# Kernel optimization log

Hardware: AMD Instinct MI355X
Metric: run time of the kernel (lower is better)

The kernel has to match this reference:

```python
import jax, jax.numpy as jnp
import numpy as np

H = W = 9
C = 16
D = 34
NHEAD = 2
HDIM = D // NHEAD  # 17
FF = 2048
NLAYERS = 2
EPS = 1e-5


def setup_inputs() -> dict:
    key = jax.random.key(0)
    ks = jax.random.split(key, 16)
    s = 0.05
    return {
        "obs": jax.random.normal(ks[0], (2, H, W), dtype=jnp.float32),
        "conv1_w": jax.random.normal(ks[1], (16, 2, 3, 3), dtype=jnp.float32) * s,
        "conv1_b": jnp.zeros((16,), jnp.float32),
        "conv2_w": jax.random.normal(ks[2], (16, 16, 3, 3), dtype=jnp.float32) * s,
        "conv2_b": jnp.zeros((16,), jnp.float32),
        "in_proj_w": jax.random.normal(ks[3], (NLAYERS, 3 * D, D), dtype=jnp.float32) * s,
        "in_proj_b": jnp.zeros((NLAYERS, 3 * D), jnp.float32),
        "out_proj_w": jax.random.normal(ks[4], (NLAYERS, D, D), dtype=jnp.float32) * s,
        "out_proj_b": jnp.zeros((NLAYERS, D), jnp.float32),
        "lin1_w": jax.random.normal(ks[5], (NLAYERS, FF, D), dtype=jnp.float32) * s,
        "lin1_b": jnp.zeros((NLAYERS, FF), jnp.float32),
        "lin2_w": jax.random.normal(ks[6], (NLAYERS, D, FF), dtype=jnp.float32) * s,
        "lin2_b": jnp.zeros((NLAYERS, D), jnp.float32),
        "ln1_g": jnp.ones((NLAYERS, D), jnp.float32),
        "ln1_b": jnp.zeros((NLAYERS, D), jnp.float32),
        "ln2_g": jnp.ones((NLAYERS, D), jnp.float32),
        "ln2_b": jnp.zeros((NLAYERS, D), jnp.float32),
    }


def _layer_norm(x, g, b):
    m = jnp.mean(x, axis=-1, keepdims=True)
    v = jnp.mean(jnp.square(x - m), axis=-1, keepdims=True)
    return (x - m) * jax.lax.rsqrt(v + EPS) * g + b


def _encoder_layer(x, ipw, ipb, opw, opb, l1w, l1b, l2w, l2b, g1, b1, g2, b2):
    # x: [S, D]. Post-norm TransformerEncoderLayer, eval mode (no dropout).
    S = x.shape[0]
    qkv = x @ ipw.T + ipb  # [S, 3D]
    q, k, v = jnp.split(qkv, 3, axis=-1)
    q = q.reshape(S, NHEAD, HDIM).transpose(1, 0, 2)  # [h, S, d]
    k = k.reshape(S, NHEAD, HDIM).transpose(1, 0, 2)
    v = v.reshape(S, NHEAD, HDIM).transpose(1, 0, 2)
    scores = jnp.einsum("hqd,hkd->hqk", q, k) / jnp.sqrt(jnp.float32(HDIM))
    attn = jax.nn.softmax(scores, axis=-1)
    o = jnp.einsum("hqk,hkd->hqd", attn, v)  # [h, S, d]
    o = o.transpose(1, 0, 2).reshape(S, D)
    o = o @ opw.T + opb
    x = _layer_norm(x + o, g1, b1)
    f = jax.nn.relu(x @ l1w.T + l1b) @ l2w.T + l2b
    return _layer_norm(x + f, g2, b2)


def _conv(x, w, b):
    y = jax.lax.conv_general_dilated(
        x, w, window_strides=(1, 1), padding="SAME",
        dimension_numbers=("NCHW", "OIHW", "NCHW"))
    return jax.nn.relu(y + b[None, :, None, None])


def reference(obs, conv1_w, conv1_b, conv2_w, conv2_b, in_proj_w, in_proj_b,
              out_proj_w, out_proj_b, lin1_w, lin1_b, lin2_w, lin2_b,
              ln1_g, ln1_b, ln2_g, ln2_b):
    x = obs[None]  # [1, 2, H, W]
    x = _conv(x, conv1_w, conv1_b)
    x = _conv(x, conv2_w, conv2_b)
    hw = H * W
    cell_emb = x[0].reshape(C, hw).T  # [hw, C]
    idx = jnp.arange(hw)
    r = (idx // W).astype(jnp.float32)
    c = (idx % W).astype(jnp.float32)
    dx = (r[:, None] - r[None, :]) / ((H - 1) / 2.0)  # [hw, hw]
    dy = (c[:, None] - c[None, :]) / ((W - 1) / 2.0)
    tok_i = jnp.broadcast_to(cell_emb[:, None, :], (hw, hw, C))
    tok_j = jnp.broadcast_to(cell_emb[None, :, :], (hw, hw, C))
    rel = jnp.stack([dx, dy], axis=-1)  # [hw, hw, 2]
    tokens = jnp.concatenate([tok_i, tok_j, rel], axis=-1).reshape(hw * hw, D)
    for l in range(NLAYERS):
        tokens = _encoder_layer(
            tokens, in_proj_w[l], in_proj_b[l], out_proj_w[l], out_proj_b[l],
            lin1_w[l], lin1_b[l], lin2_w[l], lin2_b[l],
            ln1_g[l], ln1_b[l], ln2_g[l], ln2_b[l])
    agent_idx = jnp.argmax(obs[0].reshape(-1))
    start = agent_idx * hw
    agent_tokens = jax.lax.dynamic_slice(tokens, (start, 0), (hw, D))
    return agent_tokens.mean(axis=0)  # [D]
```

## Files before the change

kernel.cpp:

```cpp
#include <hip/hip_runtime.h>
#include <hip/hip_bf16.h>

#define HH 9
#define WW 9
#define HW 81
#define CC 16
#define DD 34
#define SS 6561
#define NHEAD 2
#define HD 17
#define FF 2048
#define EPSF 1e-5f

#define NTILES 52
#define NSPLIT2 26
#define QB 64

#define NIP 7168
#define NOP 3072
#define NW1 131072
#define NW2 98304
#define NLTOT (NIP + NOP + NW1 + NW2)
#define LPREP_BLOCKS 1872
#define NKF 425984
#define NVF 212992
#define NV16 13312
#define ZERO_WORDS 332800
#define ZERO_BLOCKS 1300

#define NEAB 124416
#define NVFL1 12288
#define KSPLIT 8

typedef __attribute__((ext_vector_type(8))) short bf16x8;
typedef __attribute__((ext_vector_type(4))) float f32x4;

__device__ __forceinline__ unsigned short f2b(float f) {
  unsigned int u = __float_as_uint(f);
  u += 0x7fffu + ((u >> 16) & 1u);
  return (unsigned short)(u >> 16);
}

__global__ __launch_bounds__(256) void prep_kernel(
    const float* __restrict__ obs, const float* __restrict__ w1, const float* __restrict__ b1,
    const float* __restrict__ w2, const float* __restrict__ b2,
    float* __restrict__ cell, int* __restrict__ aidx,
    const float* __restrict__ ipw, const float* __restrict__ opw,
    const float* __restrict__ l1w, const float* __restrict__ l2w,
    unsigned short* __restrict__ ipwp, unsigned short* __restrict__ opwp,
    unsigned short* __restrict__ w1p, unsigned short* __restrict__ w2p,
    unsigned short* __restrict__ kfp, unsigned short* __restrict__ vfp,
    float* __restrict__ v16) {
  int bx = blockIdx.x;
  int t = threadIdx.x;
  if (bx == 0) {
    __shared__ float s_obs[2][11][11];
    __shared__ float s_w1[288];
    __shared__ float s_w2[2304];
    __shared__ float s_b1[16], s_b2[16];
    __shared__ float y1[CC][121];
    for (int i = t; i < 2 * 121; i += 256) ((float*)s_obs)[i] = 0.f;
    for (int i = t; i < CC * 121; i += 256) ((float*)y1)[i] = 0.f;
    for (int i = t; i < 288; i += 256) s_w1[i] = w1[i];
    for (int i = t; i < 2304; i += 256) s_w2[i] = w2[i];
    if (t < 16) { s_b1[t] = b1[t]; s_b2[t] = b2[t]; }
    __syncthreads();
    for (int i = t; i < 2 * HW; i += 256) {
      int ic = i / HW, p = i % HW;
      s_obs[ic][1 + p / WW][1 + p % WW] = obs[i];
    }
    __syncthreads();
    if (t == 0) {
      int best = 0; float bv = s_obs[0][1][1];
      for (int p = 1; p < HW; p++) {
        float v = s_obs[0][1 + p / WW][1 + p % WW];
        if (v > bv) { bv = v; best = p; }
      }
      *aidx = best;
    }
    for (int idx = t; idx < CC * HW; idx += 256) {
      int c = idx / HW, p = idx % HW;
      int i = p / WW, j = p % WW;
      float acc = s_b1[c];
#pragma unroll
      for (int ic = 0; ic < 2; ic++)
#pragma unroll
        for (int di = 0; di < 3; di++)
#pragma unroll
          for (int dj = 0; dj < 3; dj++)
            acc += s_obs[ic][i + di][j + dj] * s_w1[((c * 2 + ic) * 3 + di) * 3 + dj];
      y1[c][(i + 1) * 11 + (j + 1)] = fmaxf(acc, 0.f);
    }
    __syncthreads();
    for (int idx = t; idx < CC * HW; idx += 256) {
      int c = idx / HW, p = idx % HW;
      int i = p / WW, j = p % WW;
      float acc = s_b2[c];
#pragma unroll
      for (int ic = 0; ic < CC; ic++)
#pragma unroll
        for (int di = 0; di < 3; di++)
#pragma unroll
          for (int dj = 0; dj < 3; dj++)
            acc += y1[ic][(i + di) * 11 + (j + dj)] * s_w2[((c * CC + ic) * 3 + di) * 3 + dj];
      cell[p * CC + c] = fmaxf(acc, 0.f);
    }
  } else if (bx <= LPREP_BLOCKS) {
    int i = (bx - 1) * 256 + t;
    int layer = i / NLTOT;
    int r = i % NLTOT;
    if (r < NIP) {
      int n = r >> 6, k = r & 63;
      ipwp[layer * NIP + r] =
          (n < 102 && k < DD) ? f2b(ipw[(size_t)layer * 102 * DD + n * DD + k]) : (unsigned short)0;
    } else if (r < NIP + NOP) {
      int rr = r - NIP;
      int n = rr >> 6, k = rr & 63;
      opwp[layer * NOP + rr] =
          (n < DD && k < DD) ? f2b(opw[(size_t)layer * DD * DD + n * DD + k]) : (unsigned short)0;
    } else if (r < NIP + NOP + NW1) {
      int rr = r - NIP - NOP;
      int f = rr >> 6, k = rr & 63;
      w1p[layer * NW1 + rr] =
          (k < DD) ? f2b(l1w[(size_t)layer * FF * DD + f * DD + k]) : (unsigned short)0;
    } else {
      int rr = r - NIP - NOP - NW1;
      int d = rr >> 11, kk = rr & 2047;
      w2p[layer * NW2 + rr] =
          (d < DD) ? f2b(l2w[(size_t)layer * DD * FF + d * FF + kk]) : (unsigned short)0;
    }
  } else {
    int zi = (bx - 1 - LPREP_BLOCKS) * 256 + t;
    if (zi < NKF / 2) ((unsigned int*)kfp)[zi] = 0u;
    else if (zi < NKF / 2 + NVF / 2) ((unsigned int*)vfp)[zi - NKF / 2] = 0u;
    else if (zi < ZERO_WORDS) v16[zi - NKF / 2 - NVF / 2] = 0.f;
  }
}

__global__ __launch_bounds__(256) void ptprep_kernel(
    const float* __restrict__ cell, const float* __restrict__ ipw,
    const float* __restrict__ ipb, float* __restrict__ Pt) {
  int idx = blockIdx.x * 256 + threadIdx.x;
  if (idx >= 2 * HW * 102) return;
  int part = idx / (HW * 102);
  int rem = idx % (HW * 102);
  int a = rem / 102, n = rem % 102;
  float ra = (float)(a / WW) * 0.25f, ca = (float)(a % WW) * 0.25f;
  float acc;
  if (part == 0) {
    acc = ipb[n] + ipw[n * DD + 32] * ra + ipw[n * DD + 33] * ca;
    for (int f = 0; f < CC; f++) acc += ipw[n * DD + f] * cell[a * CC + f];
  } else {
    acc = -(ipw[n * DD + 32] * ra + ipw[n * DD + 33] * ca);
    for (int f = 0; f < CC; f++) acc += ipw[n * DD + CC + f] * cell[a * CC + f];
  }
  Pt[idx] = acc;
}

__global__ __launch_bounds__(256) void expprep_kernel(
    const float* __restrict__ Pt, float* __restrict__ eAB,
    unsigned short* __restrict__ vfragL1) {
  int idx = blockIdx.x * 256 + threadIdx.x;
  const float scale = 0.24253562503633297f;
  if (idx < NEAB) {
    int a = idx % 96; int rest = idx / 96;
    int row = rest % 81; rest /= 81;
    int ab = rest & 1, p = (rest >> 1) & 1, h = rest >> 2;
    float e = 0.f;
    if (a < HW) {
      const float* qrow = Pt + (size_t)ab * (HW * 102) + row * 102 + h * HD;
      const float* krow = Pt + (size_t)p * (HW * 102) + a * 102 + DD + h * HD;
      float dot = 0.f;
#pragma unroll
      for (int d = 0; d < HD; d++) dot += qrow[d] * krow[d];
      e = __expf(fminf(dot * scale, 40.f));
    }
    eAB[idx] = e;
  } else if (idx < NEAB + NVFL1) {
    int j = idx - NEAB;
    int a = j % 96; int rest = j / 96;
    int n = rest % 32; rest /= 32;
    int p = rest & 1, h = rest >> 1;
    float v = 0.f;
    if (a < HW) {
      if (n < HD) v = Pt[(size_t)p * (HW * 102) + a * 102 + 2 * DD + h * HD + n];
      else if (n == HD) v = 1.f;
    }
    vfragL1[((size_t)(h * 2 + p) * 32 + n) * 96 + a] = f2b(v);
  }
}

__global__ __launch_bounds__(256) void fl1_kernel(
    const float* __restrict__ cell, const float* __restrict__ eAB,
    const unsigned short* __restrict__ vfragL1,
    const unsigned short* __restrict__ opwp, const float* __restrict__ opb,
    const float* __restrict__ g1v, const float* __restrict__ b1v,
    const unsigned short* __restrict__ w1p, const unsigned short* __restrict__ w2p,
    const float* __restrict__ fb1, const float* __restrict__ fb2,
    const float* __restrict__ g2v, const float* __restrict__ b2v,
    float* __restrict__ x) {
  __shared__ __align__(16) unsigned short sE[4][16 * 96];
  __shared__ __align__(16) unsigned short soA[16 * 72];
  __shared__ float sxF[16][35];
  __shared__ __align__(16) unsigned short sxA2[16 * 72];
  __shared__ float sxF2[16][35];
  __shared__ __align__(16) unsigned short hw_[4][16 * 40];
  __shared__ float yred[4][16][49];
  int t = threadIdx.x;
  int w = t >> 6, lane = t & 63, quad = lane >> 4, col = lane & 15;
  int r0 = blockIdx.x * 16;
  int nr = min(16, SS - r0);

  for (int i = t; i < 16 * 72; i += 256) { soA[i] = 0; sxA2[i] = 0; }
  for (int i = t; i < 16 * 35; i += 256) { ((float*)sxF)[i] = 0.f; ((float*)sxF2)[i] = 0.f; }
  for (int i = t; i < nr * DD; i += 256) {
    int r = i / DD, d = i - r * DD;
    int row = r0 + r;
    int ii = row / HW, jj = row - ii * HW;
    float v;
    if (d < CC) v = cell[ii * CC + d];
    else if (d < 2 * CC) v = cell[jj * CC + (d - CC)];
    else if (d == 32) v = (float)((ii / WW) - (jj / WW)) * 0.25f;
    else v = (float)((ii % WW) - (jj % WW)) * 0.25f;
    sxF[r][d] = v;
  }

  {
    int h = w >> 1, p = w & 1;
    const float* eA = eAB + ((size_t)((h * 2 + p) * 2 + 0) * 81) * 96;
    const float* eB = eAB + ((size_t)((h * 2 + p) * 2 + 1) * 81) * 96;
    int tl = lane >> 2, asub = lane & 3;
    int row = r0 + tl;
    int tc = row < SS ? row : SS - 1;
    int it = tc / HW, jt = tc - it * HW;
    const float* eAr = eA + it * 96 + asub * 24;
    const float* eBr = eB + jt * 96 + asub * 24;
    unsigned short etmp[24];
#pragma unroll
    for (int k = 0; k < 24; k++) etmp[k] = f2b(eAr[k] * eBr[k]);
    unsigned short* Eb = &sE[w][tl * 96 + asub * 24];
#pragma unroll
    for (int k = 0; k < 3; k++)
      *(bf16x8*)(Eb + k * 8) = *(bf16x8*)(etmp + k * 8);
    const unsigned short* vf = vfragL1 + (size_t)(h * 2 + p) * 32 * 96;
    f32x4 acc0 = {0.f, 0.f, 0.f, 0.f}, acc1 = {0.f, 0.f, 0.f, 0.f};
#pragma unroll
    for (int c = 0; c < 3; c++) {
      bf16x8 ea = *(const bf16x8*)&sE[w][col * 96 + c * 32 + quad * 8];
      bf16x8 vb0 = *(const bf16x8*)&vf[col * 96 + c * 32 + quad * 8];
      bf16x8 vb1 = *(const bf16x8*)&vf[(16 + col) * 96 + c * 32 + quad * 8];
      acc0 = __builtin_amdgcn_mfma_f32_16x16x32_bf16(ea, vb0, acc0, 0, 0, 0);
      acc1 = __builtin_amdgcn_mfma_f32_16x16x32_bf16(ea, vb1, acc1, 0, 0, 0);
    }
    float Sr[4];
#pragma unroll
    for (int r = 0; r < 4; r++) Sr[r] = __shfl(acc1[r], (lane & 48) + 1);
#pragma unroll
    for (int r = 0; r < 4; r++) {
      int rr = quad * 4 + r;
      float inv = 1.f / Sr[r];
      yred[w][rr][col] = acc0[r] * inv;
      if (col == 0) yred[w][rr][16] = acc1[r] * inv;
    }
  }
  __syncthreads();
  for (int i = t; i < 16 * DD; i += 256) {
    int r = i / DD, dd = i - r * DD;
    int h2 = dd / HD, d2 = dd - h2 * HD;
    soA[r * 72 + dd] = f2b(yred[2 * h2][r][d2] + yred[2 * h2 + 1][r][d2]);
  }
  __syncthreads();

  if (w == 0) {
    bf16x8 a0 = *(const bf16x8*)&soA[col * 72 + quad * 8];
    bf16x8 a1 = *(const bf16x8*)&soA[col * 72 + 32 + quad * 8];
    f32x4 y[3];
#pragma unroll
    for (int nt = 0; nt < 3; nt++) {
      int n = nt * 16 + col;
      bf16x8 b0 = *(const bf16x8*)&opwp[n * 64 + quad * 8];
      bf16x8 b1 = *(const bf16x8*)&opwp[n * 64 + 32 + quad * 8];
      f32x4 acc = {0.f, 0.f, 0.f, 0.f};
      acc = __builtin_amdgcn_mfma_f32_16x16x32_bf16(a0, b0, acc, 0, 0, 0);
      y[nt] = __builtin_amdgcn_mfma_f32_16x16x32_bf16(a1, b1, acc, 0, 0, 0);
    }
    float yv[3][4];
    float s1[4] = {0.f, 0.f, 0.f, 0.f}, s2[4] = {0.f, 0.f, 0.f, 0.f};
#pragma unroll
    for (int nt = 0; nt < 3; nt++) {
      int d = nt * 16 + col;
      bool vd = d < DD;
      float ob = vd ? opb[d] : 0.f;
#pragma unroll
      for (int r = 0; r < 4; r++) {
        int row = quad * 4 + r;
        float v = vd ? (y[nt][r] + ob + sxF[row][d]) : 0.f;
        yv[nt][r] = v;
        s1[r] += v;
        s2[r] += v * v;
      }
    }
#pragma unroll
    for (int msk = 1; msk <= 8; msk <<= 1)
#pragma unroll
      for (int r = 0; r < 4; r++) {
        s1[r] += __shfl_xor(s1[r], msk);
        s2[r] += __shfl_xor(s2[r], msk);
      }
#pragma unroll
    for (int r = 0; r < 4; r++) {
      int row = quad * 4 + r;
      float mean = s1[r] * (1.f / DD);
      float var = s2[r] * (1.f / DD) - mean * mean;
      float rs = rsqrtf(var + EPSF);
#pragma unroll
      for (int nt = 0; nt < 3; nt++) {
        int d = nt * 16 + col;
        if (d < DD) {
          float o = (yv[nt][r] - mean) * rs * g1v[d] + b1v[d];
          sxF2[row][d] = o;
          sxA2[row * 72 + d] = f2b(o);
        }
      }
    }
  }
  __syncthreads();

  bf16x8 a0 = *(const bf16x8*)&sxA2[col * 72 + quad * 8];
  bf16x8 a1 = *(const bf16x8*)&sxA2[col * 72 + 32 + quad * 8];
  unsigned short* myh = &hw_[w][0];
  f32x4 acc3[3];
#pragma unroll
  for (int nt = 0; nt < 3; nt++) acc3[nt] = (f32x4){0.f, 0.f, 0.f, 0.f};
  for (int kt = 0; kt < 16; kt++) {
    int fbase = kt * 128 + w * 32;
#pragma unroll
    for (int nt = 0; nt < 2; nt++) {
      int f = fbase + nt * 16 + col;
      bf16x8 b0f = *(const bf16x8*)&w1p[f * 64 + quad * 8];
      bf16x8 b1f = *(const bf16x8*)&w1p[f * 64 + 32 + quad * 8];
      f32x4 hacc = {0.f, 0.f, 0.f, 0.f};
      hacc = __builtin_amdgcn_mfma_f32_16x16x32_bf16(a0, b0f, hacc, 0, 0, 0);
      hacc = __builtin_amdgcn_mfma_f32_16x16x32_bf16(a1, b1f, hacc, 0, 0, 0);
      float bias = fb1[f];
#pragma unroll
      for (int r = 0; r < 4; r++) {
        float hv = fmaxf(hacc[r] + bias, 0.f);
        myh[(quad * 4 + r) * 40 + nt * 16 + col] = f2b(hv);
      }
    }
    bf16x8 pa = *(const bf16x8*)&myh[col * 40 + quad * 8];
#pragma unroll
    for (int nt = 0; nt < 3; nt++) {
      int n = nt * 16 + col;
      bf16x8 wb = *(const bf16x8*)&w2p[(size_t)n * FF + fbase + quad * 8];
      acc3[nt] = __builtin_amdgcn_mfma_f32_16x16x32_bf16(pa, wb, acc3[nt], 0, 0, 0);
    }
  }
#pragma unroll
  for (int nt = 0; nt < 3; nt++)
#pragma unroll
    for (int r = 0; r < 4; r++)
      yred[w][quad * 4 + r][nt * 16 + col] = acc3[nt][r];
  __syncthreads();
  if (w == 0) {
    float yv[3][4];
    float s1[4] = {0.f, 0.f, 0.f, 0.f}, s2[4] = {0.f, 0.f, 0.f, 0.f};
#pragma unroll
    for (int nt = 0; nt < 3; nt++) {
      int d = nt * 16 + col;
      bool valid = d < DD;
      float b2x = valid ? fb2[d] : 0.f;
#pragma unroll
      for (int r = 0; r < 4; r++) {
        int row = quad * 4 + r;
        float v = yred[0][row][nt * 16 + col] + yred[1][row][nt * 16 + col]
                + yred[2][row][nt * 16 + col] + yred[3][row][nt * 16 + col];
        v = valid ? (v + b2x + sxF2[row][d]) : 0.f;
        yv[nt][r] = v;
        s1[r] += v;
        s2[r] += v * v;
      }
    }
#pragma unroll
    for (int msk = 1; msk <= 8; msk <<= 1)
#pragma unroll
      for (int r = 0; r < 4; r++) {
        s1[r] += __shfl_xor(s1[r], msk);
        s2[r] += __shfl_xor(s2[r], msk);
      }
#pragma unroll
    for (int r = 0; r < 4; r++) {
      int row = quad * 4 + r;
      if (row >= nr) continue;
      float mean = s1[r] * (1.f / DD);
      float var = s2[r] * (1.f / DD) - mean * mean;
      float rs = rsqrtf(var + EPSF);
#pragma unroll
      for (int nt = 0; nt < 3; nt++) {
        int d = nt * 16 + col;
        if (d < DD)
          x[(size_t)(r0 + row) * DD + d] = (yv[nt][r] - mean) * rs * g2v[d] + b2v[d];
      }
    }
  }
}

__global__ __launch_bounds__(256) void qkv2_kernel(
    const float* __restrict__ x, const unsigned short* __restrict__ ipwp,
    const float* __restrict__ ipb, const int* __restrict__ abase,
    float* __restrict__ qkv, unsigned short* __restrict__ kfp,
    unsigned short* __restrict__ vfp, float* __restrict__ v16) {
  __shared__ __align__(16) unsigned short sxA[32 * 72];
  int t = threadIdx.x;
  int w = t >> 6, lane = t & 63, quad = lane >> 4, col = lane & 15;
  int m0 = (w & 1) * 16, half = w >> 1;
  bool qpart = blockIdx.x >= 206;
  int row0 = qpart ? (abase[0] * HW + (blockIdx.x - 206) * 32) : blockIdx.x * 32;
  int nr = min(32, SS - row0);
  for (int i = t; i < 32 * 72; i += 256) sxA[i] = 0;
  __syncthreads();
  for (int i = t; i < nr * DD; i += 256) {
    int r = i / DD, d = i - r * DD;
    sxA[r * 72 + d] = f2b(x[(size_t)(row0 + r) * DD + d]);
  }
  __syncthreads();
  bf16x8 a0 = *(const bf16x8*)&sxA[(m0 + col) * 72 + quad * 8];
  bf16x8 a1 = *(const bf16x8*)&sxA[(m0 + col) * 72 + 32 + quad * 8];
  if (!qpart) {
    int ntc = half ? 2 : 3;
    for (int nt2 = 0; nt2 < ntc; nt2++) {
      int nt = half * 3 + nt2;
      int n = DD + nt * 16 + col;
      int nc = n < 112 ? n : 111;
      bf16x8 b0 = *(const bf16x8*)&ipwp[nc * 64 + quad * 8];
      bf16x8 b1 = *(const bf16x8*)&ipwp[nc * 64 + 32 + quad * 8];
      f32x4 acc = {0.f, 0.f, 0.f, 0.f};
      acc = __builtin_amdgcn_mfma_f32_16x16x32_bf16(a0, b0, acc, 0, 0, 0);
      acc = __builtin_amdgcn_mfma_f32_16x16x32_bf16(a1, b1, acc, 0, 0, 0);
      if (n < 102) {
        float bias = ipb[n];
        int kd = n - DD;
#pragma unroll
        for (int r = 0; r < 4; r++) {
          int m = m0 + quad * 4 + r;
          if (m >= nr) continue;
          int tok = row0 + m;
          float val = acc[r] + bias;
          int T = tok >> 7, tl = tok & 127;
          if (kd < 2 * HD) {
            int h = kd >= HD;
            int d = kd - h * HD;
            int colf = tl >> 3, ntk = tl & 7;
            kfp[(((size_t)h * NTILES + T) * 8 + ntk) * 512 +
                ((d >> 3) * 16 + colf) * 8 + (d & 7)] = f2b(val);
          } else {
            int vd = kd - 2 * HD;
            int h = vd >= HD;
            int d = vd - h * HD;
            if (d < 16) {
              int c = tl >> 5, qf = (tl >> 3) & 3, j = tl & 7;
              vfp[(((size_t)h * NTILES + T) * 4 + c) * 512 +
                  (qf * 16 + d) * 8 + j] = f2b(val);
            } else {
              v16[(size_t)h * (NTILES * 128) + tok] = val;
            }
          }
        }
      }
    }
  } else {
    int ntc = half ? 1 : 2;
    for (int nt2 = 0; nt2 < ntc; nt2++) {
      int nt = half * 2 + nt2;
      int n = nt * 16 + col;
      bf16x8 b0 = *(const bf16x8*)&ipwp[n * 64 + quad * 8];
      bf16x8 b1 = *(const bf16x8*)&ipwp[n * 64 + 32 + quad * 8];
      f32x4 acc = {0.f, 0.f, 0.f, 0.f};
      acc = __builtin_amdgcn_mfma_f32_16x16x32_bf16(a0, b0, acc, 0, 0, 0);
      acc = __builtin_amdgcn_mfma_f32_16x16x32_bf16(a1, b1, acc, 0, 0, 0);
      if (n < DD) {
        float bias = ipb[n];
#pragma unroll
        for (int r = 0; r < 4; r++) {
          int m = row0 + m0 + quad * 4 + r;
          if (m < SS) qkv[(size_t)m * 102 + n] = acc[r] + bias;
        }
      }
    }
  }
}

__global__ __launch_bounds__(256) void attn2_kernel(
    const float* __restrict__ qkv, const unsigned short* __restrict__ kfp,
    const unsigned short* __restrict__ vfp, const float* __restrict__ v16,
    const int* __restrict__ abase,
    float* __restrict__ opart, float* __restrict__ lpart) {
  __shared__ __align__(16) unsigned short scb[4][16 * 136];
  int t = threadIdx.x, w = t >> 6, lane = t & 63, quad = lane >> 4, col = lane & 15;
  int h = blockIdx.y, sp = blockIdx.z;
  int base = abase[0] * HW;
  int q0 = blockIdx.x * QB;
  const float scale = 0.24253562503633297f;
  const unsigned short* kf = kfp + (size_t)h * (NTILES * 8 * 512);
  const unsigned short* vf = vfp + (size_t)h * (NTILES * 4 * 512);
  const float* v16h = v16 + (size_t)h * (NTILES * 128);
  unsigned short* myscb = &scb[w][0];

  int mq = base + q0 + w * 16 + col;
  int qc = mq < SS ? mq : SS - 1;
  bf16x8 aq;
#pragma unroll
  for (int j = 0; j < 8; j++) {
    int d = quad * 8 + j;
    aq[j] = (short)((d < HD) ? f2b(qkv[(size_t)qc * 102 + h * HD + d] * scale) : 0);
  }

  f32x4 oacc = {0.f, 0.f, 0.f, 0.f};
  float o16a[4] = {0.f, 0.f, 0.f, 0.f};
  float lreg[4] = {0.f, 0.f, 0.f, 0.f};

  for (int tile = sp; tile < NTILES; tile += NSPLIT2) {
    int k0 = tile * 128;
    const unsigned short* kt = kf + (size_t)tile * (8 * 512);
    f32x4 s[8];
#pragma unroll
    for (int nt = 0; nt < 8; nt++) {
      bf16x8 kb = *(const bf16x8*)(kt + nt * 512 + lane * 8);
      f32x4 z = {0.f, 0.f, 0.f, 0.f};
      s[nt] = __builtin_amdgcn_mfma_f32_16x16x32_bf16(aq, kb, z, 0, 0, 0);
    }
    if (k0 + 128 > SS) {
#pragma unroll
      for (int nt = 0; nt < 8; nt++)
        if (k0 + col * 8 + nt >= SS) {
          s[nt][0] = -1e30f; s[nt][1] = -1e30f; s[nt][2] = -1e30f; s[nt][3] = -1e30f;
        }
    }
#pragma unroll
    for (int r = 0; r < 4; r++) {
      bf16x8 pv;
      float psl = 0.f;
#pragma unroll
      for (int nt = 0; nt < 8; nt++) {
        float p = __expf(fminf(s[nt][r], 70.f));
        s[nt][r] = p;
        psl += p;
        pv[nt] = (short)f2b(p);
      }
      lreg[r] += psl;
      *(bf16x8*)(myscb + (quad * 4 + r) * 136 + col * 8) = pv;
    }
    f32x4 va = *(const f32x4*)(v16h + k0 + col * 8);
    f32x4 vb4 = *(const f32x4*)(v16h + k0 + col * 8 + 4);
#pragma unroll
    for (int r = 0; r < 4; r++) {
      o16a[r] += s[0][r] * va[0] + s[1][r] * va[1] + s[2][r] * va[2] + s[3][r] * va[3]
               + s[4][r] * vb4[0] + s[5][r] * vb4[1] + s[6][r] * vb4[2] + s[7][r] * vb4[3];
    }
    const unsigned short* vt = vf + (size_t)tile * (4 * 512);
#pragma unroll
    for (int c = 0; c < 4; c++) {
      bf16x8 pa = *(const bf16x8*)(myscb + col * 136 + c * 32 + quad * 8);
      bf16x8 vbf = *(const bf16x8*)(vt + c * 512 + lane * 8);
      oacc = __builtin_amdgcn_mfma_f32_16x16x32_bf16(pa, vbf, oacc, 0, 0, 0);
    }
  }
#pragma unroll
  for (int msk = 1; msk <= 8; msk <<= 1)
#pragma unroll
    for (int r = 0; r < 4; r++) {
      o16a[r] += __shfl_xor(o16a[r], msk);
      lreg[r] += __shfl_xor(lreg[r], msk);
    }
  size_t obase = ((size_t)sp * NHEAD + h) * 128;
#pragma unroll
  for (int r = 0; r < 4; r++) {
    int ql = q0 + w * 16 + quad * 4 + r;
    if (ql < HW) {
      opart[(obase + ql) * HD + col] = oacc[r];
      if (col == 0) {
        opart[(obase + ql) * HD + 16] = o16a[r];
        lpart[obase + ql] = lreg[r];
      }
    }
  }
}

__global__ __launch_bounds__(256) void fl2a_kernel(
    const float* __restrict__ opart, const float* __restrict__ lpart,
    const unsigned short* __restrict__ opwp, const float* __restrict__ opb,
    const float* __restrict__ g1v, const float* __restrict__ b1v,
    const unsigned short* __restrict__ w1p, const unsigned short* __restrict__ w2p,
    const float* __restrict__ fb1, const int* __restrict__ abase,
    const float* __restrict__ x, float* __restrict__ xln, float* __restrict__ ypart) {
  __shared__ __align__(16) unsigned short soA[16 * 72];
  __shared__ float sxF[16][35];
  __shared__ __align__(16) unsigned short sxA2[16 * 72];
  __shared__ float sxF2[16][35];
  __shared__ __align__(16) unsigned short hw_[4][16 * 40];
  __shared__ float yred[4][16][49];
  int t = threadIdx.x;
  int w = t >> 6, lane = t & 63, quad = lane >> 4, col = lane & 15;
  int sp = blockIdx.y;
  int base = abase[0] * HW;
  int ql0 = blockIdx.x * 16;
  int nr = min(16, HW - ql0);
  int r0 = base + ql0;

  for (int i = t; i < 16 * 72; i += 256) { soA[i] = 0; sxA2[i] = 0; }
  for (int i = t; i < 16 * 35; i += 256) { ((float*)sxF)[i] = 0.f; ((float*)sxF2)[i] = 0.f; }
  __syncthreads();
  for (int i = t; i < nr * DD; i += 256) {
    int r = i / DD, rem = i - r * DD;
    sxF[r][rem] = x[(size_t)(r0 + r) * DD + rem];
    int ql = ql0 + r;
    int h = rem / HD, d = rem - h * HD;
    float L = 0.f, O = 0.f;
#pragma unroll
    for (int s = 0; s < NSPLIT2; s++) {
      L += lpart[((size_t)s * NHEAD + h) * 128 + ql];
      O += opart[(((size_t)s * NHEAD + h) * 128 + ql) * HD + d];
    }
    soA[r * 72 + rem] = f2b(O / L);
  }
  __syncthreads();
  if (w == 0) {
    bf16x8 a0 = *(const bf16x8*)&soA[col * 72 + quad * 8];
    bf16x8 a1 = *(const bf16x8*)&soA[col * 72 + 32 + quad * 8];
    f32x4 y[3];
#pragma unroll
    for (int nt = 0; nt < 3; nt++) {
      int n = nt * 16 + col;
      bf16x8 b0 = *(const bf16x8*)&opwp[n * 64 + quad * 8];
      bf16x8 b1 = *(const bf16x8*)&opwp[n * 64 + 32 + quad * 8];
      f32x4 acc = {0.f, 0.f, 0.f, 0.f};
      acc = __builtin_amdgcn_mfma_f32_16x16x32_bf16(a0, b0, acc, 0, 0, 0);
      y[nt] = __builtin_amdgcn_mfma_f32_16x16x32_bf16(a1, b1, acc, 0, 0, 0);
    }
    float yv[3][4];
    float s1[4] = {0.f, 0.f, 0.f, 0.f}, s2[4] = {0.f, 0.f, 0.f, 0.f};
#pragma unroll
    for (int nt = 0; nt < 3; nt++) {
      int d = nt * 16 + col;
      bool vd = d < DD;
      float ob = vd ? opb[d] : 0.f;
#pragma unroll
      for (int r = 0; r < 4; r++) {
        int row = quad * 4 + r;
        float v = vd ? (y[nt][r] + ob + sxF[row][d]) : 0.f;
        yv[nt][r] = v;
        s1[r] += v;
        s2[r] += v * v;
      }
    }
#pragma unroll
    for (int msk = 1; msk <= 8; msk <<= 1)
#pragma unroll
      for (int r = 0; r < 4; r++) {
        s1[r] += __shfl_xor(s1[r], msk);
        s2[r] += __shfl_xor(s2[r], msk);
      }
#pragma unroll
    for (int r = 0; r < 4; r++) {
      int row = quad * 4 + r;
      float mean = s1[r] * (1.f / DD);
      float var = s2[r] * (1.f / DD) - mean * mean;
      float rs = rsqrtf(var + EPSF);
#pragma unroll
      for (int nt = 0; nt < 3; nt++) {
        int d = nt * 16 + col;
        if (d < DD) {
          float o = (yv[nt][r] - mean) * rs * g1v[d] + b1v[d];
          sxF2[row][d] = o;
          sxA2[row * 72 + d] = f2b(o);
          if (sp == 0 && row < nr)
            xln[(size_t)(ql0 + row) * DD + d] = o;
        }
      }
    }
  }
  __syncthreads();
  bf16x8 a0 = *(const bf16x8*)&sxA2[col * 72 + quad * 8];
  bf16x8 a1 = *(const bf16x8*)&sxA2[col * 72 + 32 + quad * 8];
  unsigned short* myh = &hw_[w][0];
  f32x4 acc3[3];
#pragma unroll
  for (int nt = 0; nt < 3; nt++) acc3[nt] = (f32x4){0.f, 0.f, 0.f, 0.f};
  for (int kt2 = 0; kt2 < 2; kt2++) {
    int kt = sp * 2 + kt2;
    int fbase = kt * 128 + w * 32;
#pragma unroll
    for (int nt = 0; nt < 2; nt++) {
      int f = fbase + nt * 16 + col;
      bf16x8 b0f = *(const bf16x8*)&w1p[f * 64 + quad * 8];
      bf16x8 b1f = *(const bf16x8*)&w1p[f * 64 + 32 + quad * 8];
      f32x4 hacc = {0.f, 0.f, 0.f, 0.f};
      hacc = __builtin_amdgcn_mfma_f32_16x16x32_bf16(a0, b0f, hacc, 0, 0, 0);
      hacc = __builtin_amdgcn_mfma_f32_16x16x32_bf16(a1, b1f, hacc, 0, 0, 0);
      float bias = fb1[f];
#pragma unroll
      for (int r = 0; r < 4; r++) {
        float hv = fmaxf(hacc[r] + bias, 0.f);
        myh[(quad * 4 + r) * 40 + nt * 16 + col] = f2b(hv);
      }
    }
    bf16x8 pa = *(const bf16x8*)&myh[col * 40 + quad * 8];
#pragma unroll
    for (int nt = 0; nt < 3; nt++) {
      int n = nt * 16 + col;
      bf16x8 wb = *(const bf16x8*)&w2p[(size_t)n * FF + fbase + quad * 8];
      acc3[nt] = __builtin_amdgcn_mfma_f32_16x16x32_bf16(pa, wb, acc3[nt], 0, 0, 0);
    }
  }
#pragma unroll
  for (int nt = 0; nt < 3; nt++)
#pragma unroll
    for (int r = 0; r < 4; r++)
      yred[w][quad * 4 + r][nt * 16 + col] = acc3[nt][r];
  __syncthreads();
  if (w == 0) {
    for (int i = lane; i < nr * DD; i += 64) {
      int r = i / DD, d = i - r * DD;
      float v = yred[0][r][d] + yred[1][r][d] + yred[2][r][d] + yred[3][r][d];
      ypart[((size_t)sp * HW + ql0 + r) * DD + d] = v;
    }
  }
}

__global__ __launch_bounds__(256) void fl2b_kernel(
    const float* __restrict__ ypart, const float* __restrict__ xln,
    const float* __restrict__ fb2, const float* __restrict__ g2v,
    const float* __restrict__ b2v, const int* __restrict__ abase,
    float* __restrict__ x) {
  int t = threadIdx.x;
  int row = blockIdx.x * 32 + (t >> 3);
  int s8 = t & 7;
  if (row >= HW) return;
  int base = abase[0] * HW;
  float yv[5];
  float s1 = 0.f, s2 = 0.f;
  int cnt = 0;
  for (int d = s8; d < DD; d += 8) {
    float v = fb2[d] + xln[(size_t)row * DD + d];
#pragma unroll
    for (int sp = 0; sp < KSPLIT; sp++)
      v += ypart[((size_t)sp * HW + row) * DD + d];
    yv[cnt++] = v;
    s1 += v;
    s2 += v * v;
  }
  s1 += __shfl_xor(s1, 1); s2 += __shfl_xor(s2, 1);
  s1 += __shfl_xor(s1, 2); s2 += __shfl_xor(s2, 2);
  s1 += __shfl_xor(s1, 4); s2 += __shfl_xor(s2, 4);
  float mean = s1 * (1.f / DD);
  float var = s2 * (1.f / DD) - mean * mean;
  float rs = rsqrtf(var + EPSF);
  cnt = 0;
  for (int d = s8; d < DD; d += 8)
    x[(size_t)(base + row) * DD + d] = (yv[cnt++] - mean) * rs * g2v[d] + b2v[d];
}

__global__ __launch_bounds__(64) void final_kernel(
    const float* __restrict__ x, const int* __restrict__ aidx, float* __restrict__ out) {
  int d = threadIdx.x;
  if (d >= DD) return;
  int start = (*aidx) * HW;
  float acc = 0.f;
  for (int j = 0; j < HW; j++) acc += x[(size_t)(start + j) * DD + d];
  out[d] = acc * (1.f / HW);
}

extern "C" void kernel_launch(void* const* d_in, const int* in_sizes, int n_in,
                              void* d_out, int out_size, void* d_ws, size_t ws_size,
                              hipStream_t stream) {
  const float* obs = (const float*)d_in[0];
  const float* c1w = (const float*)d_in[1];
  const float* c1b = (const float*)d_in[2];
  const float* c2w = (const float*)d_in[3];
  const float* c2b = (const float*)d_in[4];
  const float* ipw = (const float*)d_in[5];
  const float* ipb = (const float*)d_in[6];
  const float* opw = (const float*)d_in[7];
  const float* opb = (const float*)d_in[8];
  const float* l1w = (const float*)d_in[9];
  const float* l1b = (const float*)d_in[10];
  const float* l2w = (const float*)d_in[11];
  const float* l2b = (const float*)d_in[12];
  const float* g1 = (const float*)d_in[13];
  const float* b1 = (const float*)d_in[14];
  const float* g2 = (const float*)d_in[15];
  const float* b2 = (const float*)d_in[16];
  float* out = (float*)d_out;

  float* ws = (float*)d_ws;
  size_t off = 0;
  float* x     = ws + off; off += SS * DD;
  float* qkv   = ws + off; off += SS * 102;
  float* cell  = ws + off; off += HW * CC;
  int*   aidx  = (int*)(ws + off); off += 1;
  off = (off + 3) & ~(size_t)3;
  float* Pt    = ws + off; off += 2 * HW * 102;
  float* opart = ws + off; off += (size_t)NSPLIT2 * NHEAD * 128 * HD;
  float* lpart = ws + off; off += (size_t)NSPLIT2 * NHEAD * 128;
  float* eAB   = ws + off; off += NEAB;
  float* xln   = ws + off; off += HW * DD;
  float* ypart = ws + off; off += (size_t)KSPLIT * HW * DD;
  off = (off + 3) & ~(size_t)3;
  unsigned short* vfragL1 = (unsigned short*)(ws + off); off += NVFL1 / 2;
  unsigned short* kfp  = (unsigned short*)(ws + off); off += NKF / 2;
  unsigned short* vfp  = (unsigned short*)(ws + off); off += NVF / 2;
  float* v16 = ws + off; off += NV16;
  unsigned short* ipwp = (unsigned short*)(ws + off); off += 2 * NIP / 2;
  unsigned short* opwp = (unsigned short*)(ws + off); off += 2 * NOP / 2;
  unsigned short* w1p  = (unsigned short*)(ws + off); off += 2 * NW1 / 2;
  unsigned short* w2p  = (unsigned short*)(ws + off); off += 2 * NW2 / 2;

  const int prep_grid = 1 + LPREP_BLOCKS + ZERO_BLOCKS;
  const int pt_blocks = (2 * HW * 102 + 255) / 256;
  const int exp_blocks = (NEAB + NVFL1 + 255) / 256;
  const int fl1_blocks = (SS + 15) / 16;

  prep_kernel<<<prep_grid, 256, 0, stream>>>(
      obs, c1w, c1b, c2w, c2b, cell, aidx,
      ipw, opw, l1w, l2w, ipwp, opwp, w1p, w2p, kfp, vfp, v16);
  ptprep_kernel<<<pt_blocks, 256, 0, stream>>>(cell, ipw, ipb, Pt);
  expprep_kernel<<<exp_blocks, 256, 0, stream>>>(Pt, eAB, vfragL1);
  fl1_kernel<<<fl1_blocks, 256, 0, stream>>>(
      cell, eAB, vfragL1, opwp, opb, g1, b1, w1p, w2p, l1b, l2b, g2, b2, x);
  qkv2_kernel<<<210, 256, 0, stream>>>(
      x, ipwp + NIP, ipb + 102, aidx, qkv, kfp, vfp, v16);
  dim3 a2g(2, NHEAD, NSPLIT2);
  attn2_kernel<<<a2g, 256, 0, stream>>>(qkv, kfp, vfp, v16, aidx, opart, lpart);
  dim3 f2g(6, KSPLIT);
  fl2a_kernel<<<f2g, 256, 0, stream>>>(
      opart, lpart, opwp + NOP, opb + DD, g1 + DD, b1 + DD,
      w1p + NW1, w2p + NW2, l1b + FF, aidx, x, xln, ypart);
  fl2b_kernel<<<3, 256, 0, stream>>>(
      ypart, xln, l2b + DD, g2 + DD, b2 + DD, aidx, x);
  final_kernel<<<1, 64, 0, stream>>>(x, aidx, out);
}
```

Before: 187.5 us.

## Widen layer-2 grids and reduce attention partials with atomics

Layer-2 attention now gives each block one key tile instead of striding over two, and accumulates unnormalized outputs and row sums into a zeroed buffer with atomicAdd. This removes the partial buffers and the 26-way reduction in fl2a. The QKV projection uses 16-row blocks, doubling its grid, and the FFN K-split doubles from 8 to 16 so each block handles one 128-wide chunk. The cost is atomic contention on a small output buffer, float summation order that is no longer deterministic, more partial sums for fl2b to reduce, and extra zeroing in prep.

```diff
diff --git a/kernel.cpp b/kernel.cpp
--- a/kernel.cpp
+++ b/kernel.cpp
@@ -13,7 +13,6 @@
 #define EPSF 1e-5f
 
 #define NTILES 52
-#define NSPLIT2 26
 #define QB 64
 
 #define NIP 7168
@@ -25,12 +24,13 @@
 #define NKF 425984
 #define NVF 212992
 #define NV16 13312
-#define ZERO_WORDS 332800
-#define ZERO_BLOCKS 1300
+#define NOSUM 4608
+#define ZERO_WORDS 337408
+#define ZERO_BLOCKS 1318
 
 #define NEAB 124416
 #define NVFL1 12288
-#define KSPLIT 8
+#define KSPLIT 16
 
 typedef __attribute__((ext_vector_type(8))) short bf16x8;
 typedef __attribute__((ext_vector_type(4))) float f32x4;
@@ -50,7 +50,7 @@
     unsigned short* __restrict__ ipwp, unsigned short* __restrict__ opwp,
     unsigned short* __restrict__ w1p, unsigned short* __restrict__ w2p,
     unsigned short* __restrict__ kfp, unsigned short* __restrict__ vfp,
-    float* __restrict__ v16) {
+    float* __restrict__ v16, float* __restrict__ osum) {
   int bx = blockIdx.x;
   int t = threadIdx.x;
   if (bx == 0) {
@@ -133,7 +133,8 @@
     int zi = (bx - 1 - LPREP_BLOCKS) * 256 + t;
     if (zi < NKF / 2) ((unsigned int*)kfp)[zi] = 0u;
     else if (zi < NKF / 2 + NVF / 2) ((unsigned int*)vfp)[zi - NKF / 2] = 0u;
-    else if (zi < ZERO_WORDS) v16[zi - NKF / 2 - NVF / 2] = 0.f;
+    else if (zi < NKF / 2 + NVF / 2 + NV16) v16[zi - NKF / 2 - NVF / 2] = 0.f;
+    else if (zi < ZERO_WORDS) osum[zi - NKF / 2 - NVF / 2 - NV16] = 0.f;
   }
 }
 
@@ -411,26 +412,25 @@
     const float* __restrict__ ipb, const int* __restrict__ abase,
     float* __restrict__ qkv, unsigned short* __restrict__ kfp,
     unsigned short* __restrict__ vfp, float* __restrict__ v16) {
-  __shared__ __align__(16) unsigned short sxA[32 * 72];
+  __shared__ __align__(16) unsigned short sxA[16 * 72];
   int t = threadIdx.x;
   int w = t >> 6, lane = t & 63, quad = lane >> 4, col = lane & 15;
-  int m0 = (w & 1) * 16, half = w >> 1;
-  bool qpart = blockIdx.x >= 206;
-  int row0 = qpart ? (abase[0] * HW + (blockIdx.x - 206) * 32) : blockIdx.x * 32;
-  int nr = min(32, SS - row0);
-  for (int i = t; i < 32 * 72; i += 256) sxA[i] = 0;
+  bool qpart = blockIdx.x >= 411;
+  int row0 = qpart ? (abase[0] * HW + (blockIdx.x - 411) * 16) : blockIdx.x * 16;
+  int nr = min(16, SS - row0);
+  for (int i = t; i < 16 * 72; i += 256) sxA[i] = 0;
   __syncthreads();
   for (int i = t; i < nr * DD; i += 256) {
     int r = i / DD, d = i - r * DD;
     sxA[r * 72 + d] = f2b(x[(size_t)(row0 + r) * DD + d]);
   }
   __syncthreads();
-  bf16x8 a0 = *(const bf16x8*)&sxA[(m0 + col) * 72 + quad * 8];
-  bf16x8 a1 = *(const bf16x8*)&sxA[(m0 + col) * 72 + 32 + quad * 8];
+  bf16x8 a0 = *(const bf16x8*)&sxA[col * 72 + quad * 8];
+  bf16x8 a1 = *(const bf16x8*)&sxA[col * 72 + 32 + quad * 8];
   if (!qpart) {
-    int ntc = half ? 2 : 3;
-    for (int nt2 = 0; nt2 < ntc; nt2++) {
-      int nt = half * 3 + nt2;
+    int npass = (w == 0) ? 2 : 1;
+    for (int pass = 0; pass < npass; pass++) {
+      int nt = (pass == 0) ? w : 4;
       int n = DD + nt * 16 + col;
       int nc = n < 112 ? n : 111;
       bf16x8 b0 = *(const bf16x8*)&ipwp[nc * 64 + quad * 8];
@@ -443,7 +443,7 @@
         int kd = n - DD;
 #pragma unroll
         for (int r = 0; r < 4; r++) {
-          int m = m0 + quad * 4 + r;
+          int m = quad * 4 + r;
           if (m >= nr) continue;
           int tok = row0 + m;
           float val = acc[r] + bias;
@@ -470,10 +470,8 @@
       }
     }
   } else {
-    int ntc = half ? 1 : 2;
-    for (int nt2 = 0; nt2 < ntc; nt2++) {
-      int nt = half * 2 + nt2;
-      int n = nt * 16 + col;
+    if (w < 3) {
+      int n = w * 16 + col;
       bf16x8 b0 = *(const bf16x8*)&ipwp[n * 64 + quad * 8];
       bf16x8 b1 = *(const bf16x8*)&ipwp[n * 64 + 32 + quad * 8];
       f32x4 acc = {0.f, 0.f, 0.f, 0.f};
@@ -483,7 +481,7 @@
         float bias = ipb[n];
 #pragma unroll
         for (int r = 0; r < 4; r++) {
-          int m = row0 + m0 + quad * 4 + r;
+          int m = row0 + quad * 4 + r;
           if (m < SS) qkv[(size_t)m * 102 + n] = acc[r] + bias;
         }
       }
@@ -494,11 +492,11 @@
 __global__ __launch_bounds__(256) void attn2_kernel(
     const float* __restrict__ qkv, const unsigned short* __restrict__ kfp,
     const unsigned short* __restrict__ vfp, const float* __restrict__ v16,
-    const int* __restrict__ abase,
-    float* __restrict__ opart, float* __restrict__ lpart) {
+    const int* __restrict__ abase, float* __restrict__ o_sum, float* __restrict__ l_sum) {
   __shared__ __align__(16) unsigned short scb[4][16 * 136];
   int t = threadIdx.x, w = t >> 6, lane = t & 63, quad = lane >> 4, col = lane & 15;
-  int h = blockIdx.y, sp = blockIdx.z;
+  int h = blockIdx.y;
+  int tile = blockIdx.z;
   int base = abase[0] * HW;
   int q0 = blockIdx.x * QB;
   const float scale = 0.24253562503633297f;
@@ -516,55 +514,52 @@
     aq[j] = (short)((d < HD) ? f2b(qkv[(size_t)qc * 102 + h * HD + d] * scale) : 0);
   }
 
+  int k0 = tile * 128;
+  const unsigned short* kt = kf + (size_t)tile * (8 * 512);
+  f32x4 s[8];
+#pragma unroll
+  for (int nt = 0; nt < 8; nt++) {
+    bf16x8 kb = *(const bf16x8*)(kt + nt * 512 + lane * 8);
+    f32x4 z = {0.f, 0.f, 0.f, 0.f};
+    s[nt] = __builtin_amdgcn_mfma_f32_16x16x32_bf16(aq, kb, z, 0, 0, 0);
+  }
+  if (k0 + 128 > SS) {
+#pragma unroll
+    for (int nt = 0; nt < 8; nt++)
+      if (k0 + col * 8 + nt >= SS) {
+        s[nt][0] = -1e30f; s[nt][1] = -1e30f; s[nt][2] = -1e30f; s[nt][3] = -1e30f;
+      }
+  }
+  float lreg[4];
+#pragma unroll
+  for (int r = 0; r < 4; r++) {
+    bf16x8 pv;
+    float psl = 0.f;
+#pragma unroll
+    for (int nt = 0; nt < 8; nt++) {
+      float p = __expf(fminf(s[nt][r], 70.f));
+      s[nt][r] = p;
+      psl += p;
+      pv[nt] = (short)f2b(p);
+    }
+    lreg[r] = psl;
+    *(bf16x8*)(myscb + (quad * 4 + r) * 136 + col * 8) = pv;
+  }
+  float o16a[4];
+  f32x4 va = *(const f32x4*)(v16h + k0 + col * 8);
+  f32x4 vb4 = *(const f32x4*)(v16h + k0 + col * 8 + 4);
+#pragma unroll
+  for (int r = 0; r < 4; r++) {
+    o16a[r] = s[0][r] * va[0] + s[1][r] * va[1] + s[2][r] * va[2] + s[3][r] * va[3]
+            + s[4][r] * vb4[0] + s[5][r] * vb4[1] + s[6][r] * vb4[2] + s[7][r] * vb4[3];
+  }
   f32x4 oacc = {0.f, 0.f, 0.f, 0.f};
-  float o16a[4] = {0.f, 0.f, 0.f, 0.f};
-  float lreg[4] = {0.f, 0.f, 0.f, 0.f};
-
-  for (int tile = sp; tile < NTILES; tile += NSPLIT2) {
-    int k0 = tile * 128;
-    const unsigned short* kt = kf + (size_t)tile * (8 * 512);
-    f32x4 s[8];
-#pragma unroll
-    for (int nt = 0; nt < 8; nt++) {
-      bf16x8 kb = *(const bf16x8*)(kt + nt * 512 + lane * 8);
-      f32x4 z = {0.f, 0.f, 0.f, 0.f};
-      s[nt] = __builtin_amdgcn_mfma_f32_16x16x32_bf16(aq, kb, z, 0, 0, 0);
-    }
-    if (k0 + 128 > SS) {
-#pragma unroll
-      for (int nt = 0; nt < 8; nt++)
-        if (k0 + col * 8 + nt >= SS) {
-          s[nt][0] = -1e30f; s[nt][1] = -1e30f; s[nt][2] = -1e30f; s[nt][3] = -1e30f;
-        }
-    }
-#pragma unroll
-    for (int r = 0; r < 4; r++) {
-      bf16x8 pv;
-      float psl = 0.f;
-#pragma unroll
-      for (int nt = 0; nt < 8; nt++) {
-        float p = __expf(fminf(s[nt][r], 70.f));
-        s[nt][r] = p;
-        psl += p;
-        pv[nt] = (short)f2b(p);
-      }
-      lreg[r] += psl;
-      *(bf16x8*)(myscb + (quad * 4 + r) * 136 + col * 8) = pv;
-    }
-    f32x4 va = *(const f32x4*)(v16h + k0 + col * 8);
-    f32x4 vb4 = *(const f32x4*)(v16h + k0 + col * 8 + 4);
-#pragma unroll
-    for (int r = 0; r < 4; r++) {
-      o16a[r] += s[0][r] * va[0] + s[1][r] * va[1] + s[2][r] * va[2] + s[3][r] * va[3]
-               + s[4][r] * vb4[0] + s[5][r] * vb4[1] + s[6][r] * vb4[2] + s[7][r] * vb4[3];
-    }
-    const unsigned short* vt = vf + (size_t)tile * (4 * 512);
-#pragma unroll
-    for (int c = 0; c < 4; c++) {
-      bf16x8 pa = *(const bf16x8*)(myscb + col * 136 + c * 32 + quad * 8);
-      bf16x8 vbf = *(const bf16x8*)(vt + c * 512 + lane * 8);
-      oacc = __builtin_amdgcn_mfma_f32_16x16x32_bf16(pa, vbf, oacc, 0, 0, 0);
-    }
+  const unsigned short* vt = vf + (size_t)tile * (4 * 512);
+#pragma unroll
+  for (int c = 0; c < 4; c++) {
+    bf16x8 pa = *(const bf16x8*)(myscb + col * 136 + c * 32 + quad * 8);
+    bf16x8 vbf = *(const bf16x8*)(vt + c * 512 + lane * 8);
+    oacc = __builtin_amdgcn_mfma_f32_16x16x32_bf16(pa, vbf, oacc, 0, 0, 0);
   }
 #pragma unroll
   for (int msk = 1; msk <= 8; msk <<= 1)
@@ -573,22 +568,21 @@
       o16a[r] += __shfl_xor(o16a[r], msk);
       lreg[r] += __shfl_xor(lreg[r], msk);
     }
-  size_t obase = ((size_t)sp * NHEAD + h) * 128;
 #pragma unroll
   for (int r = 0; r < 4; r++) {
     int ql = q0 + w * 16 + quad * 4 + r;
     if (ql < HW) {
-      opart[(obase + ql) * HD + col] = oacc[r];
+      atomicAdd(&o_sum[(size_t)ql * DD + h * HD + col], oacc[r]);
       if (col == 0) {
-        opart[(obase + ql) * HD + 16] = o16a[r];
-        lpart[obase + ql] = lreg[r];
+        atomicAdd(&o_sum[(size_t)ql * DD + h * HD + 16], o16a[r]);
+        atomicAdd(&l_sum[h * 128 + ql], lreg[r]);
       }
     }
   }
 }
 
 __global__ __launch_bounds__(256) void fl2a_kernel(
-    const float* __restrict__ opart, const float* __restrict__ lpart,
+    const float* __restrict__ o_sum, const float* __restrict__ l_sum,
     const unsigned short* __restrict__ opwp, const float* __restrict__ opb,
     const float* __restrict__ g1v, const float* __restrict__ b1v,
     const unsigned short* __restrict__ w1p, const unsigned short* __restrict__ w2p,
@@ -597,7 +591,6 @@
   __shared__ __align__(16) unsigned short soA[16 * 72];
   __shared__ float sxF[16][35];
   __shared__ __align__(16) unsigned short sxA2[16 * 72];
-  __shared__ float sxF2[16][35];
   __shared__ __align__(16) unsigned short hw_[4][16 * 40];
   __shared__ float yred[4][16][49];
   int t = threadIdx.x;
@@ -609,19 +602,15 @@
   int r0 = base + ql0;
 
   for (int i = t; i < 16 * 72; i += 256) { soA[i] = 0; sxA2[i] = 0; }
-  for (int i = t; i < 16 * 35; i += 256) { ((float*)sxF)[i] = 0.f; ((float*)sxF2)[i] = 0.f; }
+  for (int i = t; i < 16 * 35; i += 256) ((float*)sxF)[i] = 0.f;
   __syncthreads();
   for (int i = t; i < nr * DD; i += 256) {
     int r = i / DD, rem = i - r * DD;
     sxF[r][rem] = x[(size_t)(r0 + r) * DD + rem];
     int ql = ql0 + r;
-    int h = rem / HD, d = rem - h * HD;
-    float L = 0.f, O = 0.f;
-#pragma unroll
-    for (int s = 0; s < NSPLIT2; s++) {
-      L += lpart[((size_t)s * NHEAD + h) * 128 + ql];
-      O += opart[(((size_t)s * NHEAD + h) * 128 + ql) * HD + d];
-    }
+    int h = rem / HD;
+    float L = l_sum[h * 128 + ql];
+    float O = o_sum[(size_t)ql * DD + rem];
     soA[r * 72 + rem] = f2b(O / L);
   }
   __syncthreads();
@@ -672,7 +661,6 @@
         int d = nt * 16 + col;
         if (d < DD) {
           float o = (yv[nt][r] - mean) * rs * g1v[d] + b1v[d];
-          sxF2[row][d] = o;
           sxA2[row * 72 + d] = f2b(o);
           if (sp == 0 && row < nr)
             xln[(size_t)(ql0 + row) * DD + d] = o;
@@ -687,9 +675,8 @@
   f32x4 acc3[3];
 #pragma unroll
   for (int nt = 0; nt < 3; nt++) acc3[nt] = (f32x4){0.f, 0.f, 0.f, 0.f};
-  for (int kt2 = 0; kt2 < 2; kt2++) {
-    int kt = sp * 2 + kt2;
-    int fbase = kt * 128 + w * 32;
+  {
+    int fbase = sp * 128 + w * 32;
 #pragma unroll
     for (int nt = 0; nt < 2; nt++) {
       int f = fbase + nt * 16 + col;
@@ -801,8 +788,6 @@
   int*   aidx  = (int*)(ws + off); off += 1;
   off = (off + 3) & ~(size_t)3;
   float* Pt    = ws + off; off += 2 * HW * 102;
-  float* opart = ws + off; off += (size_t)NSPLIT2 * NHEAD * 128 * HD;
-  float* lpart = ws + off; off += (size_t)NSPLIT2 * NHEAD * 128;
   float* eAB   = ws + off; off += NEAB;
   float* xln   = ws + off; off += HW * DD;
   float* ypart = ws + off; off += (size_t)KSPLIT * HW * DD;
@@ -811,6 +796,8 @@
   unsigned short* kfp  = (unsigned short*)(ws + off); off += NKF / 2;
   unsigned short* vfp  = (unsigned short*)(ws + off); off += NVF / 2;
   float* v16 = ws + off; off += NV16;
+  float* o_sum = ws + off; off += 128 * DD;
+  float* l_sum = ws + off; off += 256;
   unsigned short* ipwp = (unsigned short*)(ws + off); off += 2 * NIP / 2;
   unsigned short* opwp = (unsigned short*)(ws + off); off += 2 * NOP / 2;
   unsigned short* w1p  = (unsigned short*)(ws + off); off += 2 * NW1 / 2;
@@ -823,18 +810,18 @@
 
   prep_kernel<<<prep_grid, 256, 0, stream>>>(
       obs, c1w, c1b, c2w, c2b, cell, aidx,
-      ipw, opw, l1w, l2w, ipwp, opwp, w1p, w2p, kfp, vfp, v16);
+      ipw, opw, l1w, l2w, ipwp, opwp, w1p, w2p, kfp, vfp, v16, o_sum);
   ptprep_kernel<<<pt_blocks, 256, 0, stream>>>(cell, ipw, ipb, Pt);
   expprep_kernel<<<exp_blocks, 256, 0, stream>>>(Pt, eAB, vfragL1);
   fl1_kernel<<<fl1_blocks, 256, 0, stream>>>(
       cell, eAB, vfragL1, opwp, opb, g1, b1, w1p, w2p, l1b, l2b, g2, b2, x);
-  qkv2_kernel<<<210, 256, 0, stream>>>(
+  qkv2_kernel<<<419, 256, 0, stream>>>(
       x, ipwp + NIP, ipb + 102, aidx, qkv, kfp, vfp, v16);
-  dim3 a2g(2, NHEAD, NSPLIT2);
-  attn2_kernel<<<a2g, 256, 0, stream>>>(qkv, kfp, vfp, v16, aidx, opart, lpart);
+  dim3 a2g(2, NHEAD, NTILES);
+  attn2_kernel<<<a2g, 256, 0, stream>>>(qkv, kfp, vfp, v16, aidx, o_sum, l_sum);
   dim3 f2g(6, KSPLIT);
   fl2a_kernel<<<f2g, 256, 0, stream>>>(
-      opart, lpart, opwp + NOP, opb + DD, g1 + DD, b1 + DD,
+      o_sum, l_sum, opwp + NOP, opb + DD, g1 + DD, b1 + DD,
       w1p + NW1, w2p + NW2, l1b + FF, aidx, x, xln, ypart);
   fl2b_kernel<<<3, 256, 0, stream>>>(
       ypart, xln, l2b + DD, g2 + DD, b2 + DD, aidx, x);
```

Result: faster. 181.7 us (median of 2 runs) (-3.1%).
